# Optimization experiments

Hardware: AMD Instinct MI355X
Metric: run time of the kernel (lower is better)

The kernel has to match this reference:

```python
import jax, jax.numpy as jnp
import numpy as np
import math

EPS = 1e-5

def _ln(x, g, b):
    m = jnp.mean(x, axis=-1, keepdims=True)
    v = jnp.mean((x - m) ** 2, axis=-1, keepdims=True)
    return (x - m) * jax.lax.rsqrt(v + EPS) * g + b

def _heads(t, H):
    B, T, C = t.shape
    return t.reshape(B, T, H, C // H).transpose(0, 2, 1, 3)  # [B,H,T,D]

def _merge(t):
    B, H, T, D = t.shape
    return t.transpose(0, 2, 1, 3).reshape(B, T, H * D)

def _self_attn(x, w, b, pw, pb, H):
    B, T, C = x.shape
    q, k, v = jnp.split(x @ w + b, 3, axis=-1)
    q, k, v = _heads(q, H), _heads(k, H), _heads(v, H)
    D = C // H
    att = jnp.einsum('bhqd,bhkd->bhqk', q, k) * (1.0 / math.sqrt(D))
    causal = jnp.tril(jnp.ones((T, T), bool))
    att = jnp.where(causal[None, None], att, jnp.float32(-jnp.inf))
    att = jax.nn.softmax(att, axis=-1)
    out = _merge(jnp.einsum('bhqk,bhkd->bhqd', att, v))
    return out @ pw + pb

def _cross_attn(enc, dec, w, b, pw, pb, H):
    B, Td, C = dec.shape
    q_dec = jnp.split(dec @ w + b, 3, axis=-1)[0]
    _, k_enc, v_enc = jnp.split(enc @ w + b, 3, axis=-1)
    q = _heads(q_dec, H); k = _heads(k_enc, H); v = _heads(v_enc, H)
    D = C // H
    att = jnp.einsum('bhqd,bhkd->bhqk', q, k) * (1.0 / math.sqrt(D))
    att = jax.nn.softmax(att, axis=-1)
    out = _merge(jnp.einsum('bhqk,bhkd->bhqd', att, v))
    return out @ pw + pb

def _block(x, encoder_embd,
           ln1_g, ln1_b, ln2_g, ln2_b, ln3_g, ln3_b,
           attn_w, attn_b, aproj_w, aproj_b,
           ca_w, ca_b, caproj_w, caproj_b,
           fc_w, fc_b, mproj_w, mproj_b,
           down_w, down_b, up_w, up_b, H=16):
    x = x + _self_attn(_ln(x, ln1_g, ln1_b), attn_w, attn_b, aproj_w, aproj_b, H)
    x = x + _cross_attn(encoder_embd, _ln(x, ln2_g, ln2_b), ca_w, ca_b, caproj_w, caproj_b, H)
    h = jax.nn.gelu(_ln(x, ln3_g, ln3_b) @ fc_w + fc_b, approximate=True) @ mproj_w + mproj_b
    adapt = jax.nn.gelu(h @ down_w + down_b, approximate=True) @ up_w + up_b + h  # Adapter residual
    return x + adapt


def setup_inputs() -> dict:
    key = jax.random.key(0)
    ks = jax.random.split(key, 12)
    B, T, Te, C, H = 4, 1024, 257, 1024, 16
    s = 0.02
    f32 = jnp.float32
    return {
        'x': jax.random.normal(ks[0], (B, T, C), f32),
        'encoder_embd': jax.random.normal(ks[1], (B, Te, C), f32),
        'prefix_embd': jnp.zeros((B, 1, C), f32),
        'ln1_g': jnp.ones((C,), f32), 'ln1_b': jnp.zeros((C,), f32),
        'ln2_g': jnp.ones((C,), f32), 'ln2_b': jnp.zeros((C,), f32),
        'ln3_g': jnp.ones((C,), f32), 'ln3_b': jnp.zeros((C,), f32),
        'attn_w': jax.random.normal(ks[2], (C, 3 * C), f32) * s,
        'attn_b': jnp.zeros((3 * C,), f32),
        'aproj_w': jax.random.normal(ks[3], (C, C), f32) * s,
        'aproj_b': jnp.zeros((C,), f32),
        'ca_w': jax.random.normal(ks[4], (C, 3 * C), f32) * s,
        'ca_b': jnp.zeros((3 * C,), f32),
        'caproj_w': jax.random.normal(ks[5], (C, C), f32) * s,
        'caproj_b': jnp.zeros((C,), f32),
        'fc_w': jax.random.normal(ks[6], (C, 4 * C), f32) * s,
        'fc_b': jnp.zeros((4 * C,), f32),
        'mproj_w': jax.random.normal(ks[7], (4 * C, C), f32) * s,
        'mproj_b': jnp.zeros((C,), f32),
        'down_w': jax.random.normal(ks[8], (C, C // 4), f32) * s,
        'down_b': jnp.zeros((C // 4,), f32),
        'up_w': jax.random.normal(ks[9], (C // 4, C), f32) * s,
        'up_b': jnp.zeros((C,), f32),
    }


def reference(x, encoder_embd, prefix_embd,
              ln1_g, ln1_b, ln2_g, ln2_b, ln3_g, ln3_b,
              attn_w, attn_b, aproj_w, aproj_b,
              ca_w, ca_b, caproj_w, caproj_b,
              fc_w, fc_b, mproj_w, mproj_b,
              down_w, down_b, up_w, up_b):
    # prefix_embd unused (peft='adapter')
    return _block(x, encoder_embd,
                  ln1_g, ln1_b, ln2_g, ln2_b, ln3_g, ln3_b,
                  attn_w, attn_b, aproj_w, aproj_b,
                  ca_w, ca_b, caproj_w, caproj_b,
                  fc_w, fc_b, mproj_w, mproj_b,
                  down_w, down_b, up_w, up_b)
```

## Files before the change

### kernel.cpp

```cpp
#include <hip/hip_runtime.h>

typedef __attribute__((ext_vector_type(8))) short short8v;
typedef __attribute__((ext_vector_type(8))) unsigned short ushort8v;
typedef __attribute__((ext_vector_type(4))) unsigned short ushort4v;
typedef __attribute__((ext_vector_type(4))) float f32x4;

__device__ __forceinline__ unsigned short f2b(float f) {
  unsigned int u = __float_as_uint(f);
  unsigned int r = (u + 0x7FFFu + ((u >> 16) & 1u)) >> 16;
  return (unsigned short)r;
}
__device__ __forceinline__ float b2f(unsigned short h) {
  return __uint_as_float(((unsigned int)h) << 16);
}
__device__ __forceinline__ float gelu_f(float x) {
  float z = 0.7978845608028654f * (x + 0.044715f * x * x * x);
  float e = __expf(2.0f * z);
  float t = 1.0f - 2.0f / (e + 1.0f);
  return 0.5f * x * (1.0f + t);
}
__device__ __forceinline__ int xcd_swz(int wgid, int nwg) {
  int q = nwg >> 3, r = nwg & 7;
  int xcd = wgid & 7, idx = wgid >> 3;
  return (xcd < r ? xcd * (q + 1) : r * (q + 1) + (xcd - r) * q) + idx;
}
__device__ __forceinline__ void map_tile(int wgid, int nwg, int nbx, int& tm, int& tn) {
  int nby = nwg / nbx;
  if ((nwg & 7) == 0 && (nby & 3) == 0 && (nbx & 1) == 0) {
    int x = wgid & 7, idx = wgid >> 3;
    int rh = nby >> 2, rw = nbx >> 1;
    int xr = x >> 1, xc = x & 1;
    tm = xr * rh + idx / rw;
    tn = xc * rw + idx % rw;
  } else {
    int swz = xcd_swz(wgid, nwg);
    tm = swz / nbx;
    tn = swz % nbx;
  }
}

__global__ __launch_bounds__(256) void k_wprep(
    const float* aw, unsigned short* awt,
    const float* apw, unsigned short* apwt,
    const float* cw, unsigned short* cwt,
    const float* cpw, unsigned short* cpwt,
    const float* fw, unsigned short* fwt,
    const float* mw, unsigned short* mwt,
    const float* dw, unsigned short* dwt,
    const float* uw, unsigned short* uwt,
    const float* enc, unsigned short* encb) {
  __shared__ float tile[64][65];
  int bid = blockIdx.x, t = threadIdx.x;
  const float* w; unsigned short* wt; int K, N, gx, l;
  if      (bid < 768)  { w = aw;  wt = awt;  K = 1024; N = 3072; gx = 48; l = bid; }
  else if (bid < 1024) { w = apw; wt = apwt; K = 1024; N = 1024; gx = 16; l = bid - 768; }
  else if (bid < 1792) { w = cw;  wt = cwt;  K = 1024; N = 3072; gx = 48; l = bid - 1024; }
  else if (bid < 2048) { w = cpw; wt = cpwt; K = 1024; N = 1024; gx = 16; l = bid - 1792; }
  else if (bid < 3072) { w = fw;  wt = fwt;  K = 1024; N = 4096; gx = 64; l = bid - 2048; }
  else if (bid < 4096) { w = mw;  wt = mwt;  K = 4096; N = 1024; gx = 16; l = bid - 3072; }
  else if (bid < 4160) { w = dw;  wt = dwt;  K = 1024; N = 256;  gx = 4;  l = bid - 4096; }
  else if (bid < 4224) { w = uw;  wt = uwt;  K = 256;  N = 1024; gx = 16; l = bid - 4160; }
  else {
    size_t i = ((size_t)(bid - 4224) * 256 + t) * 4;
    f32x4 v = *(const f32x4*)&enc[i];
    ushort4v o;
#pragma unroll
    for (int j = 0; j < 4; ++j) o[j] = f2b(v[j]);
    *(ushort4v*)&encb[i] = o;
    return;
  }
  int bx = l % gx, by = l / gx;
  int tn = bx * 64, tk = by * 64;
  int c = t & 63, r0 = t >> 6;
#pragma unroll
  for (int p = 0; p < 16; ++p) {
    int r = r0 + p * 4;
    tile[r][c] = w[(size_t)(tk + r) * N + tn + c];
  }
  __syncthreads();
#pragma unroll
  for (int p = 0; p < 16; ++p) {
    int r = r0 + p * 4;
    wt[(size_t)(tn + r) * K + tk + c] = f2b(tile[c][r]);
  }
}

__global__ __launch_bounds__(256) void k_ln(const float* __restrict__ in,
                                            const float* __restrict__ g,
                                            const float* __restrict__ b,
                                            unsigned short* __restrict__ out) {
  int row = blockIdx.x;
  const float* x = in + (size_t)row * 1024;
  int t = threadIdx.x;
  float v0 = x[t], v1 = x[t + 256], v2 = x[t + 512], v3 = x[t + 768];
  float s = v0 + v1 + v2 + v3;
  float s2 = v0 * v0 + v1 * v1 + v2 * v2 + v3 * v3;
#pragma unroll
  for (int m = 1; m < 64; m <<= 1) { s += __shfl_xor(s, m); s2 += __shfl_xor(s2, m); }
  __shared__ float rs[4], rs2[4];
  int w = t >> 6;
  if ((t & 63) == 0) { rs[w] = s; rs2[w] = s2; }
  __syncthreads();
  s = rs[0] + rs[1] + rs[2] + rs[3];
  s2 = rs2[0] + rs2[1] + rs2[2] + rs2[3];
  float mean = s * (1.0f / 1024.0f);
  float var = s2 * (1.0f / 1024.0f) - mean * mean;
  float rinv = rsqrtf(var + 1e-5f);
  unsigned short* o = out + (size_t)row * 1024;
  o[t]       = f2b((v0 - mean) * rinv * g[t]       + b[t]);
  o[t + 256] = f2b((v1 - mean) * rinv * g[t + 256] + b[t + 256]);
  o[t + 512] = f2b((v2 - mean) * rinv * g[t + 512] + b[t + 512]);
  o[t + 768] = f2b((v3 - mean) * rinv * g[t + 768] + b[t + 768]);
}

template <bool GELU, bool WF32, bool WBF16, int NRES, bool RES1B>
__global__ __launch_bounds__(256, 2) void k_g128b(
    const unsigned short* __restrict__ A, int lda,
    const unsigned short* __restrict__ W, int ldw,
    const float* __restrict__ bias,
    const float* __restrict__ res1, const unsigned short* __restrict__ res1b,
    const float* __restrict__ res2,
    float* __restrict__ outF, unsigned short* __restrict__ outB,
    int M, int N, int K, int nbx) {
  __shared__ unsigned short lds[32768];
  const int t = threadIdx.x;
  int tm, tn;
  map_tile(blockIdx.x, gridDim.x, nbx, tm, tn);
  const int tileM = tm * 128, tileN = tn * 128;
  const int lane = t & 63, w = t >> 6;
  const int wm = (w >> 1) * 64, wn = (w & 1) * 64;
  const int lr16 = lane & 15, kc4 = lane >> 4;

  const int sr = t >> 1, hb = t & 1;
  int gr = tileM + sr; if (gr >= M) gr = M - 1;
  const unsigned short* ga = A + (size_t)gr * lda + hb * 32;
  const unsigned short* gw = W + (size_t)(tileN + sr) * ldw + hb * 32;
  unsigned short* const wbA = &lds[sr * 64];
  const int wsl[4] = {((hb * 4 + 0) ^ (sr & 7)) * 8, ((hb * 4 + 1) ^ (sr & 7)) * 8,
                      ((hb * 4 + 2) ^ (sr & 7)) * 8, ((hb * 4 + 3) ^ (sr & 7)) * 8};

  f32x4 acc[4][4];
#pragma unroll
  for (int i = 0; i < 4; ++i)
#pragma unroll
    for (int j = 0; j < 4; ++j) acc[i][j] = f32x4{0.f, 0.f, 0.f, 0.f};

  const int nt = K >> 7;
  ushort8v ra[8], rb[8];

#define LOADT(T)                                                    \
  do {                                                              \
    int ko = (T) << 7;                                              \
    _Pragma("unroll") for (int j = 0; j < 4; ++j) {                 \
      ra[j]     = *(const ushort8v*)(ga + ko + j * 8);              \
      ra[4 + j] = *(const ushort8v*)(ga + ko + 64 + j * 8);         \
      rb[j]     = *(const ushort8v*)(gw + ko + j * 8);              \
      rb[4 + j] = *(const ushort8v*)(gw + ko + 64 + j * 8);         \
    }                                                               \
  } while (0)
#define WRITET()                                                    \
  do {                                                              \
    _Pragma("unroll") for (int j = 0; j < 4; ++j) {                 \
      *(ushort8v*)(wbA + wsl[j])         = ra[j];                   \
      *(ushort8v*)(wbA + 8192 + wsl[j])  = ra[4 + j];               \
      *(ushort8v*)(wbA + 16384 + wsl[j]) = rb[j];                   \
      *(ushort8v*)(wbA + 24576 + wsl[j]) = rb[4 + j];               \
    }                                                               \
  } while (0)
#define COMPUTE(hsel)                                                           \
  do {                                                                          \
    const int ba = (hsel) * 8192, bb = 16384 + (hsel) * 8192;                   \
    _Pragma("unroll") for (int ks = 0; ks < 2; ++ks) {                          \
      short8v bfr[4];                                                           \
      _Pragma("unroll") for (int n = 0; n < 4; ++n) {                           \
        int r = wn + n * 16 + lr16;                                             \
        int sl = ((ks * 4 + kc4) ^ (r & 7)) * 8;                                \
        bfr[n] = *(const short8v*)&lds[bb + r * 64 + sl];                       \
      }                                                                         \
      _Pragma("unroll") for (int mi = 0; mi < 4; ++mi) {                        \
        int r = wm + mi * 16 + lr16;                                            \
        int sl = ((ks * 4 + kc4) ^ (r & 7)) * 8;                                \
        short8v af = *(const short8v*)&lds[ba + r * 64 + sl];                   \
        _Pragma("unroll") for (int n = 0; n < 4; ++n)                           \
          acc[mi][n] =                                                          \
              __builtin_amdgcn_mfma_f32_16x16x32_bf16(af, bfr[n], acc[mi][n], 0, 0, 0); \
      }                                                                         \
    }                                                                           \
  } while (0)

  LOADT(0);
  WRITET();
  __syncthreads();

  for (int T = 0; T < nt; ++T) {
    if (T + 1 < nt) LOADT(T + 1);
    COMPUTE(0);
    COMPUTE(1);
    __syncthreads();
    if (T + 1 < nt) {
      WRITET();
      __syncthreads();
    }
  }
#undef LOADT
#undef WRITET
#undef COMPUTE

#pragma unroll
  for (int mi = 0; mi < 4; ++mi) {
#pragma unroll
    for (int n = 0; n < 4; ++n) {
      int col = tileN + wn + n * 16 + lr16;
      float bv = bias[col];
#pragma unroll
      for (int qi = 0; qi < 4; ++qi) {
        int row = tileM + wm + mi * 16 + kc4 * 4 + qi;
        if (row < M) {
          float v = acc[mi][n][qi] + bv;
          if (GELU) v = gelu_f(v);
          size_t o = (size_t)row * N + col;
          if (NRES >= 1) v += RES1B ? b2f(res1b[o]) : res1[o];
          if (NRES >= 2) v += res2[o];
          if (WF32) outF[o] = v;
          if (WBF16) outB[o] = f2b(v);
        }
      }
    }
  }
}

__global__ __launch_bounds__(256) void k_vtrans(const unsigned short* __restrict__ src,
                                                int src_stride, int src_off, int TB,
                                                unsigned short* __restrict__ dst, int dst_tstride) {
  __shared__ unsigned short tile[64][72];
  int tb = blockIdx.x, bh = blockIdx.y;
  int b = bh >> 4, h = bh & 15;
  int t = threadIdx.x;
  int r = t >> 2, c0 = (t & 3) * 16;
  int tok = tb * 64 + r; if (tok >= TB) tok = TB - 1;
  const unsigned short* s = src + (size_t)(b * TB + tok) * src_stride + src_off + h * 64 + c0;
  *(ushort8v*)&tile[r][c0] = *(const ushort8v*)s;
  *(ushort8v*)&tile[r][c0 + 8] = *(const ushort8v*)(s + 8);
  __syncthreads();
  unsigned short tmp[16];
#pragma unroll
  for (int j = 0; j < 16; ++j) tmp[j] = tile[c0 + j][r];
  unsigned short* dp = dst + ((size_t)bh * 64 + r) * dst_tstride + tb * 64 + c0;
  *(ushort8v*)dp = *(const ushort8v*)&tmp[0];
  *(ushort8v*)(dp + 8) = *(const ushort8v*)&tmp[8];
}

template <bool CAUSAL>
__global__ __launch_bounds__(256) void k_attn(
    const unsigned short* __restrict__ Qb, int q_stride,
    const unsigned short* __restrict__ Kb, int k_stride, int k_off, int TKR,
    const unsigned short* __restrict__ Vt, int vt_tstride,
    unsigned short* __restrict__ out, int Tk) {
  __shared__ unsigned short Kl[64 * 72];
  __shared__ unsigned short Vl[64 * 72];
  __shared__ unsigned short Pl[4][16 * 72];
  const int swz = xcd_swz(blockIdx.x, gridDim.x);
  int qb = swz & 15, bh = swz >> 4;
  int b = bh >> 4, h = bh & 15;
  int t = threadIdx.x, lane = t & 63, w = t >> 6;
  int g = lane >> 4, lc = lane & 15;

  int qrow_g = qb * 64 + w * 16 + lc;
  const unsigned short* qp = Qb + (size_t)(b * 1024 + qrow_g) * q_stride + h * 64 + g * 8;
  short8v aq0 = *(const short8v*)qp;
  short8v aq1 = *(const short8v*)(qp + 32);

  f32x4 o[4];
  float m_[4], l_[4];
#pragma unroll
  for (int dt = 0; dt < 4; ++dt) o[dt] = f32x4{0.f, 0.f, 0.f, 0.f};
#pragma unroll
  for (int r = 0; r < 4; ++r) { m_[r] = -3.0e38f; l_[r] = 0.0f; }

  int srow = t >> 2;
  int sc = (t & 3) * 16;
  int ntiles = CAUSAL ? (qb + 1) : ((Tk + 63) >> 6);

  for (int kt = 0; kt < ntiles; ++kt) {
    __syncthreads();
    {
      int kg = kt * 64 + srow;
      if (!CAUSAL && kg >= Tk) kg = Tk - 1;
      const unsigned short* ks = Kb + (size_t)(b * TKR + kg) * k_stride + k_off + h * 64 + sc;
      *(ushort8v*)&Kl[srow * 72 + sc]     = *(const ushort8v*)ks;
      *(ushort8v*)&Kl[srow * 72 + sc + 8] = *(const ushort8v*)(ks + 8);
      const unsigned short* vs = Vt + ((size_t)bh * 64 + srow) * vt_tstride + kt * 64 + sc;
      *(ushort8v*)&Vl[srow * 72 + sc]     = *(const ushort8v*)vs;
      *(ushort8v*)&Vl[srow * 72 + sc + 8] = *(const ushort8v*)(vs + 8);
    }
    __syncthreads();

    f32x4 s[4];
#pragma unroll
    for (int jt = 0; jt < 4; ++jt) {
      short8v bk0 = *(const short8v*)&Kl[(jt * 16 + lc) * 72 + g * 8];
      short8v bk1 = *(const short8v*)&Kl[(jt * 16 + lc) * 72 + g * 8 + 32];
      f32x4 acc = f32x4{0.f, 0.f, 0.f, 0.f};
      acc = __builtin_amdgcn_mfma_f32_16x16x32_bf16(aq0, bk0, acc, 0, 0, 0);
      acc = __builtin_amdgcn_mfma_f32_16x16x32_bf16(aq1, bk1, acc, 0, 0, 0);
      s[jt] = acc;
    }
#pragma unroll
    for (int jt = 0; jt < 4; ++jt)
#pragma unroll
      for (int r = 0; r < 4; ++r) {
        float sv = s[jt][r] * 0.125f;
        bool masked = CAUSAL ? (kt == qb && (jt * 16 + lc) > (w * 16 + g * 4 + r))
                             : (kt * 64 + jt * 16 + lc >= Tk);
        s[jt][r] = masked ? -3.0e38f : sv;
      }
    float f[4];
#pragma unroll
    for (int r = 0; r < 4; ++r) {
      float mx = fmaxf(fmaxf(s[0][r], s[1][r]), fmaxf(s[2][r], s[3][r]));
      mx = fmaxf(mx, __shfl_xor(mx, 1));
      mx = fmaxf(mx, __shfl_xor(mx, 2));
      mx = fmaxf(mx, __shfl_xor(mx, 4));
      mx = fmaxf(mx, __shfl_xor(mx, 8));
      float mnew = fmaxf(m_[r], mx);
      f[r] = __expf(m_[r] - mnew);
      m_[r] = mnew;
      float rsum = 0.0f;
#pragma unroll
      for (int jt = 0; jt < 4; ++jt) {
        float p = __expf(s[jt][r] - mnew);
        s[jt][r] = p;
        rsum += p;
      }
      rsum += __shfl_xor(rsum, 1);
      rsum += __shfl_xor(rsum, 2);
      rsum += __shfl_xor(rsum, 4);
      rsum += __shfl_xor(rsum, 8);
      l_[r] = l_[r] * f[r] + rsum;
    }
#pragma unroll
    for (int dt = 0; dt < 4; ++dt)
#pragma unroll
      for (int r = 0; r < 4; ++r) o[dt][r] *= f[r];
#pragma unroll
    for (int jt = 0; jt < 4; ++jt)
#pragma unroll
      for (int r = 0; r < 4; ++r)
        Pl[w][(g * 4 + r) * 72 + jt * 16 + lc] = f2b(s[jt][r]);
    short8v ap0 = *(const short8v*)&Pl[w][lc * 72 + g * 8];
    short8v ap1 = *(const short8v*)&Pl[w][lc * 72 + g * 8 + 32];
#pragma unroll
    for (int dt = 0; dt < 4; ++dt) {
      short8v bv0 = *(const short8v*)&Vl[(dt * 16 + lc) * 72 + g * 8];
      short8v bv1 = *(const short8v*)&Vl[(dt * 16 + lc) * 72 + g * 8 + 32];
      o[dt] = __builtin_amdgcn_mfma_f32_16x16x32_bf16(ap0, bv0, o[dt], 0, 0, 0);
      o[dt] = __builtin_amdgcn_mfma_f32_16x16x32_bf16(ap1, bv1, o[dt], 0, 0, 0);
    }
  }
  size_t orow = (size_t)(b * 1024 + qb * 64 + w * 16) * 1024 + h * 64;
#pragma unroll
  for (int r = 0; r < 4; ++r) {
    float inv = 1.0f / l_[r];
#pragma unroll
    for (int dt = 0; dt < 4; ++dt)
      out[orow + (size_t)(g * 4 + r) * 1024 + dt * 16 + lc] = f2b(o[dt][r] * inv);
  }
}

extern "C" void kernel_launch(void* const* d_in, const int* in_sizes, int n_in,
                              void* d_out, int out_size, void* d_ws, size_t ws_size,
                              hipStream_t stream) {
  (void)in_sizes; (void)n_in; (void)out_size; (void)ws_size;
  const float* x       = (const float*)d_in[0];
  const float* enc     = (const float*)d_in[1];
  const float* ln1_g   = (const float*)d_in[3];
  const float* ln1_b   = (const float*)d_in[4];
  const float* ln2_g   = (const float*)d_in[5];
  const float* ln2_b   = (const float*)d_in[6];
  const float* ln3_g   = (const float*)d_in[7];
  const float* ln3_b   = (const float*)d_in[8];
  const float* attn_w  = (const float*)d_in[9];
  const float* attn_b  = (const float*)d_in[10];
  const float* aproj_w = (const float*)d_in[11];
  const float* aproj_b = (const float*)d_in[12];
  const float* ca_w    = (const float*)d_in[13];
  const float* ca_b    = (const float*)d_in[14];
  const float* caproj_w= (const float*)d_in[15];
  const float* caproj_b= (const float*)d_in[16];
  const float* fc_w    = (const float*)d_in[17];
  const float* fc_b    = (const float*)d_in[18];
  const float* mproj_w = (const float*)d_in[19];
  const float* mproj_b = (const float*)d_in[20];
  const float* down_w  = (const float*)d_in[21];
  const float* down_b  = (const float*)d_in[22];
  const float* up_w    = (const float*)d_in[23];
  const float* up_b    = (const float*)d_in[24];
  float* out = (float*)d_out;
  char* ws = (char*)d_ws;

  const size_t O_WATTN = 0, O_WAPROJ = 6291456, O_WCA = 8388608, O_WCAPROJ = 14680064,
               O_WFC = 16777216, O_WMPROJ = 25165824, O_WDOWN = 33554432, O_WUP = 34078720,
               O_ENC = 34603008, O_LN = 36708352, O_BIG = 45096960,
               O_XRES = 78651392, O_ATTN = 112205824;

  unsigned short* wt_attn   = (unsigned short*)(ws + O_WATTN);
  unsigned short* wt_aproj  = (unsigned short*)(ws + O_WAPROJ);
  unsigned short* wt_ca     = (unsigned short*)(ws + O_WCA);
  unsigned short* wt_caproj = (unsigned short*)(ws + O_WCAPROJ);
  unsigned short* wt_fc     = (unsigned short*)(ws + O_WFC);
  unsigned short* wt_mproj  = (unsigned short*)(ws + O_WMPROJ);
  unsigned short* wt_down   = (unsigned short*)(ws + O_WDOWN);
  unsigned short* wt_up     = (unsigned short*)(ws + O_WUP);
  unsigned short* encbf     = (unsigned short*)(ws + O_ENC);
  unsigned short* lnout     = (unsigned short*)(ws + O_LN);
  unsigned short* hbf       = (unsigned short*)(ws + O_LN);
  unsigned short* qkvb      = (unsigned short*)(ws + O_BIG);
  unsigned short* vt_self   = (unsigned short*)(ws + O_BIG + 25165824);
  unsigned short* q2b       = (unsigned short*)(ws + O_BIG);
  unsigned short* kvb       = (unsigned short*)(ws + O_BIG + 8388608);
  unsigned short* vt_cross  = (unsigned short*)(ws + O_BIG + 12599296);
  unsigned short* caout     = (unsigned short*)(ws + O_BIG + 15220736);
  unsigned short* fcout     = (unsigned short*)(ws + O_BIG);
  float*          xres      = (float*)(ws + O_XRES);
  unsigned short* attnout   = (unsigned short*)(ws + O_ATTN);
  unsigned short* dmid      = (unsigned short*)(ws + O_ATTN);

  dim3 blk(256);

  k_wprep<<<dim3(5252), blk, 0, stream>>>(
      attn_w, wt_attn, aproj_w, wt_aproj, ca_w, wt_ca, caproj_w, wt_caproj,
      fc_w, wt_fc, mproj_w, wt_mproj, down_w, wt_down, up_w, wt_up, enc, encbf);

  k_ln<<<dim3(4096), blk, 0, stream>>>(x, ln1_g, ln1_b, lnout);
  k_g128b<false, false, true, 0, false><<<dim3(768), blk, 0, stream>>>(
      lnout, 1024, wt_attn, 1024, attn_b, nullptr, nullptr, nullptr, nullptr, qkvb,
      4096, 3072, 1024, 24);
  k_vtrans<<<dim3(16, 64), blk, 0, stream>>>(qkvb, 3072, 2048, 1024, vt_self, 1024);
  k_attn<true><<<dim3(1024), blk, 0, stream>>>(
      qkvb, 3072, qkvb, 3072, 1024, 1024, vt_self, 1024, attnout, 1024);
  k_g128b<false, true, false, 1, false><<<dim3(256), blk, 0, stream>>>(
      attnout, 1024, wt_aproj, 1024, aproj_b, x, nullptr, nullptr, xres, nullptr,
      4096, 1024, 1024, 8);

  k_ln<<<dim3(4096), blk, 0, stream>>>(xres, ln2_g, ln2_b, lnout);
  k_g128b<false, false, true, 0, false><<<dim3(256), blk, 0, stream>>>(
      lnout, 1024, wt_ca, 1024, ca_b, nullptr, nullptr, nullptr, nullptr, q2b,
      4096, 1024, 1024, 8);
  k_g128b<false, false, true, 0, false><<<dim3(144), blk, 0, stream>>>(
      encbf, 1024, wt_ca + (size_t)1024 * 1024, 1024, ca_b + 1024, nullptr, nullptr,
      nullptr, nullptr, kvb, 1028, 2048, 1024, 16);
  k_vtrans<<<dim3(5, 64), blk, 0, stream>>>(kvb, 2048, 1024, 257, vt_cross, 320);
  k_attn<false><<<dim3(1024), blk, 0, stream>>>(
      q2b, 1024, kvb, 2048, 0, 257, vt_cross, 320, caout, 257);
  k_g128b<false, true, false, 1, false><<<dim3(256), blk, 0, stream>>>(
      caout, 1024, wt_caproj, 1024, caproj_b, xres, nullptr, nullptr, xres, nullptr,
      4096, 1024, 1024, 8);

  k_ln<<<dim3(4096), blk, 0, stream>>>(xres, ln3_g, ln3_b, lnout);
  k_g128b<true, false, true, 0, false><<<dim3(1024), blk, 0, stream>>>(
      lnout, 1024, wt_fc, 1024, fc_b, nullptr, nullptr, nullptr, nullptr, fcout,
      4096, 4096, 1024, 32);
  k_g128b<false, false, true, 0, false><<<dim3(256), blk, 0, stream>>>(
      fcout, 4096, wt_mproj, 4096, mproj_b, nullptr, nullptr, nullptr, nullptr, hbf,
      4096, 1024, 4096, 8);

  k_g128b<true, false, true, 0, false><<<dim3(64), blk, 0, stream>>>(
      hbf, 1024, wt_down, 1024, down_b, nullptr, nullptr, nullptr, nullptr, dmid,
      4096, 256, 1024, 2);
  k_g128b<false, true, false, 2, true><<<dim3(256), blk, 0, stream>>>(
      dmid, 256, wt_up, 256, up_b, nullptr, hbf, xres, out, nullptr,
      4096, 1024, 256, 8);
}
```

Measured before the change: 474.0 us.

## Drop weight pre-transpose pass; load fp32 weights directly in GEMM with double-buffered LDS

Removes the separate kernel that transposed and converted every weight matrix to bf16. The GEMM now reads fp32 weights in their original row-major layout, converts them to bf16 in registers, and writes them swizzled into LDS. The K tile shrinks from 128 to 64 and the loop becomes double-buffered, so there is a single barrier per step. This saves a full read and write of roughly 26M weight elements per call, but each GEMM now reads twice as many weight bytes as fp32 with strided scalar loads, and every output tile repeats the bf16 conversion.

```diff
diff --git a/kernel.cpp b/kernel.cpp
--- a/kernel.cpp
+++ b/kernel.cpp
@@ -39,50 +39,14 @@
   }
 }
 
-__global__ __launch_bounds__(256) void k_wprep(
-    const float* aw, unsigned short* awt,
-    const float* apw, unsigned short* apwt,
-    const float* cw, unsigned short* cwt,
-    const float* cpw, unsigned short* cpwt,
-    const float* fw, unsigned short* fwt,
-    const float* mw, unsigned short* mwt,
-    const float* dw, unsigned short* dwt,
-    const float* uw, unsigned short* uwt,
-    const float* enc, unsigned short* encb) {
-  __shared__ float tile[64][65];
-  int bid = blockIdx.x, t = threadIdx.x;
-  const float* w; unsigned short* wt; int K, N, gx, l;
-  if      (bid < 768)  { w = aw;  wt = awt;  K = 1024; N = 3072; gx = 48; l = bid; }
-  else if (bid < 1024) { w = apw; wt = apwt; K = 1024; N = 1024; gx = 16; l = bid - 768; }
-  else if (bid < 1792) { w = cw;  wt = cwt;  K = 1024; N = 3072; gx = 48; l = bid - 1024; }
-  else if (bid < 2048) { w = cpw; wt = cpwt; K = 1024; N = 1024; gx = 16; l = bid - 1792; }
-  else if (bid < 3072) { w = fw;  wt = fwt;  K = 1024; N = 4096; gx = 64; l = bid - 2048; }
-  else if (bid < 4096) { w = mw;  wt = mwt;  K = 4096; N = 1024; gx = 16; l = bid - 3072; }
-  else if (bid < 4160) { w = dw;  wt = dwt;  K = 1024; N = 256;  gx = 4;  l = bid - 4096; }
-  else if (bid < 4224) { w = uw;  wt = uwt;  K = 256;  N = 1024; gx = 16; l = bid - 4160; }
-  else {
-    size_t i = ((size_t)(bid - 4224) * 256 + t) * 4;
-    f32x4 v = *(const f32x4*)&enc[i];
-    ushort4v o;
-#pragma unroll
-    for (int j = 0; j < 4; ++j) o[j] = f2b(v[j]);
-    *(ushort4v*)&encb[i] = o;
-    return;
-  }
-  int bx = l % gx, by = l / gx;
-  int tn = bx * 64, tk = by * 64;
-  int c = t & 63, r0 = t >> 6;
-#pragma unroll
-  for (int p = 0; p < 16; ++p) {
-    int r = r0 + p * 4;
-    tile[r][c] = w[(size_t)(tk + r) * N + tn + c];
-  }
-  __syncthreads();
-#pragma unroll
-  for (int p = 0; p < 16; ++p) {
-    int r = r0 + p * 4;
-    wt[(size_t)(tn + r) * K + tk + c] = f2b(tile[c][r]);
-  }
+__global__ __launch_bounds__(256) void k_enccvt(const float* __restrict__ enc,
+                                                unsigned short* __restrict__ encb) {
+  size_t i = ((size_t)blockIdx.x * 256 + threadIdx.x) * 4;
+  f32x4 v = *(const f32x4*)&enc[i];
+  ushort4v o;
+#pragma unroll
+  for (int j = 0; j < 4; ++j) o[j] = f2b(v[j]);
+  *(ushort4v*)&encb[i] = o;
 }
 
 __global__ __launch_bounds__(256) void k_ln(const float* __restrict__ in,
@@ -114,9 +78,9 @@
 }
 
 template <bool GELU, bool WF32, bool WBF16, int NRES, bool RES1B>
-__global__ __launch_bounds__(256, 2) void k_g128b(
+__global__ __launch_bounds__(256, 2) void k_gf(
     const unsigned short* __restrict__ A, int lda,
-    const unsigned short* __restrict__ W, int ldw,
+    const float* __restrict__ W, int ldw,
     const float* __restrict__ bias,
     const float* __restrict__ res1, const unsigned short* __restrict__ res1b,
     const float* __restrict__ res2,
@@ -134,10 +98,14 @@
   const int sr = t >> 1, hb = t & 1;
   int gr = tileM + sr; if (gr >= M) gr = M - 1;
   const unsigned short* ga = A + (size_t)gr * lda + hb * 32;
-  const unsigned short* gw = W + (size_t)(tileN + sr) * ldw + hb * 32;
-  unsigned short* const wbA = &lds[sr * 64];
-  const int wsl[4] = {((hb * 4 + 0) ^ (sr & 7)) * 8, ((hb * 4 + 1) ^ (sr & 7)) * 8,
-                      ((hb * 4 + 2) ^ (sr & 7)) * 8, ((hb * 4 + 3) ^ (sr & 7)) * 8};
+  unsigned short* const wA = &lds[sr * 64];
+  const int wslA[4] = {((hb * 4 + 0) ^ (sr & 7)) * 8, ((hb * 4 + 1) ^ (sr & 7)) * 8,
+                       ((hb * 4 + 2) ^ (sr & 7)) * 8, ((hb * 4 + 3) ^ (sr & 7)) * 8};
+  const int bn = t & 127, kg = t >> 7;
+  const float* gwf = W + tileN + bn;
+  unsigned short* const wB = &lds[8192 + bn * 64];
+  const int wslB[4] = {((kg * 4 + 0) ^ (bn & 7)) * 8, ((kg * 4 + 1) ^ (bn & 7)) * 8,
+                       ((kg * 4 + 2) ^ (bn & 7)) * 8, ((kg * 4 + 3) ^ (bn & 7)) * 8};
 
   f32x4 acc[4][4];
 #pragma unroll
@@ -145,42 +113,46 @@
 #pragma unroll
     for (int j = 0; j < 4; ++j) acc[i][j] = f32x4{0.f, 0.f, 0.f, 0.f};
 
-  const int nt = K >> 7;
-  ushort8v ra[8], rb[8];
-
-#define LOADT(T)                                                    \
-  do {                                                              \
-    int ko = (T) << 7;                                              \
-    _Pragma("unroll") for (int j = 0; j < 4; ++j) {                 \
-      ra[j]     = *(const ushort8v*)(ga + ko + j * 8);              \
-      ra[4 + j] = *(const ushort8v*)(ga + ko + 64 + j * 8);         \
-      rb[j]     = *(const ushort8v*)(gw + ko + j * 8);              \
-      rb[4 + j] = *(const ushort8v*)(gw + ko + 64 + j * 8);         \
-    }                                                               \
+  const int nt = K >> 6;
+  ushort8v ra[4];
+  float fb[32];
+
+#define LOADT(T)                                                              \
+  do {                                                                        \
+    size_t ko = (size_t)(T) << 6;                                             \
+    _Pragma("unroll") for (int j = 0; j < 4; ++j)                             \
+      ra[j] = *(const ushort8v*)(ga + ko + j * 8);                            \
+    size_t kb = (ko + kg * 32) * (size_t)ldw;                                 \
+    _Pragma("unroll") for (int j = 0; j < 32; ++j)                            \
+      fb[j] = gwf[kb + (size_t)j * ldw];                                      \
+    __builtin_amdgcn_sched_barrier(0);                                        \
   } while (0)
-#define WRITET()                                                    \
-  do {                                                              \
-    _Pragma("unroll") for (int j = 0; j < 4; ++j) {                 \
-      *(ushort8v*)(wbA + wsl[j])         = ra[j];                   \
-      *(ushort8v*)(wbA + 8192 + wsl[j])  = ra[4 + j];               \
-      *(ushort8v*)(wbA + 16384 + wsl[j]) = rb[j];                   \
-      *(ushort8v*)(wbA + 24576 + wsl[j]) = rb[4 + j];               \
-    }                                                               \
+#define WRITET(bsel)                                                          \
+  do {                                                                        \
+    unsigned short* dA = wA + (bsel) * 16384;                                 \
+    _Pragma("unroll") for (int j = 0; j < 4; ++j)                             \
+      *(ushort8v*)(dA + wslA[j]) = ra[j];                                     \
+    unsigned short* dB = wB + (bsel) * 16384;                                 \
+    _Pragma("unroll") for (int c = 0; c < 4; ++c) {                           \
+      ushort8v v;                                                             \
+      _Pragma("unroll") for (int e = 0; e < 8; ++e) v[e] = f2b(fb[c * 8 + e]);\
+      *(ushort8v*)(dB + wslB[c]) = v;                                         \
+    }                                                                         \
   } while (0)
-#define COMPUTE(hsel)                                                           \
+#define COMPUTE(bsel)                                                           \
   do {                                                                          \
-    const int ba = (hsel) * 8192, bb = 16384 + (hsel) * 8192;                   \
+    const int base = (bsel) * 16384;                                            \
     _Pragma("unroll") for (int ks = 0; ks < 2; ++ks) {                          \
       short8v bfr[4];                                                           \
       _Pragma("unroll") for (int n = 0; n < 4; ++n) {                           \
         int r = wn + n * 16 + lr16;                                             \
         int sl = ((ks * 4 + kc4) ^ (r & 7)) * 8;                                \
-        bfr[n] = *(const short8v*)&lds[bb + r * 64 + sl];                       \
+        bfr[n] = *(const short8v*)&lds[base + 8192 + r * 64 + sl];              \
       }                                                                         \
       _Pragma("unroll") for (int mi = 0; mi < 4; ++mi) {                        \
         int r = wm + mi * 16 + lr16;                                            \
         int sl = ((ks * 4 + kc4) ^ (r & 7)) * 8;                                \
-        short8v af = *(const short8v*)&lds[ba + r * 64 + sl];                   \
+        short8v af = *(const short8v*)&lds[base + r * 64 + sl];                 \
         _Pragma("unroll") for (int n = 0; n < 4; ++n)                           \
           acc[mi][n] =                                                          \
               __builtin_amdgcn_mfma_f32_16x16x32_bf16(af, bfr[n], acc[mi][n], 0, 0, 0); \
@@ -189,18 +161,14 @@
   } while (0)
 
   LOADT(0);
-  WRITET();
+  WRITET(0);
   __syncthreads();
 
   for (int T = 0; T < nt; ++T) {
     if (T + 1 < nt) LOADT(T + 1);
-    COMPUTE(0);
-    COMPUTE(1);
+    COMPUTE(T & 1);
+    if (T + 1 < nt) WRITET((T + 1) & 1);
     __syncthreads();
-    if (T + 1 < nt) {
-      WRITET();
-      __syncthreads();
-    }
   }
 #undef LOADT
 #undef WRITET
@@ -398,19 +366,9 @@
   float* out = (float*)d_out;
   char* ws = (char*)d_ws;
 
-  const size_t O_WATTN = 0, O_WAPROJ = 6291456, O_WCA = 8388608, O_WCAPROJ = 14680064,
-               O_WFC = 16777216, O_WMPROJ = 25165824, O_WDOWN = 33554432, O_WUP = 34078720,
-               O_ENC = 34603008, O_LN = 36708352, O_BIG = 45096960,
+  const size_t O_ENC = 34603008, O_LN = 36708352, O_BIG = 45096960,
                O_XRES = 78651392, O_ATTN = 112205824;
 
-  unsigned short* wt_attn   = (unsigned short*)(ws + O_WATTN);
-  unsigned short* wt_aproj  = (unsigned short*)(ws + O_WAPROJ);
-  unsigned short* wt_ca     = (unsigned short*)(ws + O_WCA);
-  unsigned short* wt_caproj = (unsigned short*)(ws + O_WCAPROJ);
-  unsigned short* wt_fc     = (unsigned short*)(ws + O_WFC);
-  unsigned short* wt_mproj  = (unsigned short*)(ws + O_WMPROJ);
-  unsigned short* wt_down   = (unsigned short*)(ws + O_WDOWN);
-  unsigned short* wt_up     = (unsigned short*)(ws + O_WUP);
   unsigned short* encbf     = (unsigned short*)(ws + O_ENC);
   unsigned short* lnout     = (unsigned short*)(ws + O_LN);
   unsigned short* hbf       = (unsigned short*)(ws + O_LN);
@@ -427,47 +385,45 @@
 
   dim3 blk(256);
 
-  k_wprep<<<dim3(5252), blk, 0, stream>>>(
-      attn_w, wt_attn, aproj_w, wt_aproj, ca_w, wt_ca, caproj_w, wt_caproj,
-      fc_w, wt_fc, mproj_w, wt_mproj, down_w, wt_down, up_w, wt_up, enc, encbf);
+  k_enccvt<<<dim3(1028), blk, 0, stream>>>(enc, encbf);
 
   k_ln<<<dim3(4096), blk, 0, stream>>>(x, ln1_g, ln1_b, lnout);
-  k_g128b<false, false, true, 0, false><<<dim3(768), blk, 0, stream>>>(
-      lnout, 1024, wt_attn, 1024, attn_b, nullptr, nullptr, nullptr, nullptr, qkvb,
+  k_gf<false, false, true, 0, false><<<dim3(768), blk, 0, stream>>>(
+      lnout, 1024, attn_w, 3072, attn_b, nullptr, nullptr, nullptr, nullptr, qkvb,
       4096, 3072, 1024, 24);
   k_vtrans<<<dim3(16, 64), blk, 0, stream>>>(qkvb, 3072, 2048, 1024, vt_self, 1024);
   k_attn<true><<<dim3(1024), blk, 0, stream>>>(
       qkvb, 3072, qkvb, 3072, 1024, 1024, vt_self, 1024, attnout, 1024);
-  k_g128b<false, true, false, 1, false><<<dim3(256), blk, 0, stream>>>(
-      attnout, 1024, wt_aproj, 1024, aproj_b, x, nullptr, nullptr, xres, nullptr,
+  k_gf<false, true, false, 1, false><<<dim3(256), blk, 0, stream>>>(
+      attnout, 1024, aproj_w, 1024, aproj_b, x, nullptr, nullptr, xres, nullptr,
       4096, 1024, 1024, 8);
 
   k_ln<<<dim3(4096), blk, 0, stream>>>(xres, ln2_g, ln2_b, lnout);
-  k_g128b<false, false, true, 0, false><<<dim3(256), blk, 0, stream>>>(
-      lnout, 1024, wt_ca, 1024, ca_b, nullptr, nullptr, nullptr, nullptr, q2b,
+  k_gf<false, false, true, 0, false><<<dim3(256), blk, 0, stream>>>(
+      lnout, 1024, ca_w, 3072, ca_b, nullptr, nullptr, nullptr, nullptr, q2b,
       4096, 1024, 1024, 8);
-  k_g128b<false, false, true, 0, false><<<dim3(144), blk, 0, stream>>>(
-      encbf, 1024, wt_ca + (size_t)1024 * 1024, 1024, ca_b + 1024, nullptr, nullptr,
+  k_gf<false, false, true, 0, false><<<dim3(144), blk, 0, stream>>>(
+      encbf, 1024, ca_w + 1024, 3072, ca_b + 1024, nullptr, nullptr,
       nullptr, nullptr, kvb, 1028, 2048, 1024, 16);
   k_vtrans<<<dim3(5, 64), blk, 0, stream>>>(kvb, 2048, 1024, 257, vt_cross, 320);
   k_attn<false><<<dim3(1024), blk, 0, stream>>>(
       q2b, 1024, kvb, 2048, 0, 257, vt_cross, 320, caout, 257);
-  k_g128b<false, true, false, 1, false><<<dim3(256), blk, 0, stream>>>(
-      caout, 1024, wt_caproj, 1024, caproj_b, xres, nullptr, nullptr, xres, nullptr,
+  k_gf<false, true, false, 1, false><<<dim3(256), blk, 0, stream>>>(
+      caout, 1024, caproj_w, 1024, caproj_b, xres, nullptr, nullptr, xres, nullptr,
       4096, 1024, 1024, 8);
 
   k_ln<<<dim3(4096), blk, 0, stream>>>(xres, ln3_g, ln3_b, lnout);
-  k_g128b<true, false, true, 0, false><<<dim3(1024), blk, 0, stream>>>(
-      lnout, 1024, wt_fc, 1024, fc_b, nullptr, nullptr, nullptr, nullptr, fcout,
+  k_gf<true, false, true, 0, false><<<dim3(1024), blk, 0, stream>>>(
+      lnout, 1024, fc_w, 4096, fc_b, nullptr, nullptr, nullptr, nullptr, fcout,
       4096, 4096, 1024, 32);
-  k_g128b<false, false, true, 0, false><<<dim3(256), blk, 0, stream>>>(
-      fcout, 4096, wt_mproj, 4096, mproj_b, nullptr, nullptr, nullptr, nullptr, hbf,
+  k_gf<false, false, true, 0, false><<<dim3(256), blk, 0, stream>>>(
+      fcout, 4096, mproj_w, 1024, mproj_b, nullptr, nullptr, nullptr, nullptr, hbf,
       4096, 1024, 4096, 8);
 
-  k_g128b<true, false, true, 0, false><<<dim3(64), blk, 0, stream>>>(
-      hbf, 1024, wt_down, 1024, down_b, nullptr, nullptr, nullptr, nullptr, dmid,
+  k_gf<true, false, true, 0, false><<<dim3(64), blk, 0, stream>>>(
+      hbf, 1024, down_w, 256, down_b, nullptr, nullptr, nullptr, nullptr, dmid,
       4096, 256, 1024, 2);
-  k_g128b<false, true, false, 2, true><<<dim3(256), blk, 0, stream>>>(
-      dmid, 256, wt_up, 256, up_b, nullptr, hbf, xres, out, nullptr,
+  k_gf<false, true, false, 2, true><<<dim3(256), blk, 0, stream>>>(
+      dmid, 256, up_w, 1024, up_b, nullptr, hbf, xres, out, nullptr,
       4096, 1024, 256, 8);
 }
```

Result: slower. 522.3 us (+10.2%).
